# Kernel tuning notes

Measured on AMD Instinct MI355X. Metric: run time of the kernel, lower is better.

The kernel has to match this reference:

```python
import jax, jax.numpy as jnp
import numpy as np
from jax import lax

B, C_IN, C_OUT, H, W = 32, 96, 96, 56, 56
E = 8          # num_experts
HID = 576      # round(96 * 6)
K = 3          # depthwise kernel size


def setup_inputs() -> dict:
    key = jax.random.key(0)
    ks = jax.random.split(key, 12)
    f = lambda k, s, sc=0.05: jax.random.normal(k, s, dtype=jnp.float32) * sc
    return {
        "x": jax.random.normal(ks[0], (B, C_IN, H, W), dtype=jnp.float32),
        # router for expand conv (input = x, C_IN channels)
        "w_r1": f(ks[1], (E, C_IN)), "b_r1": jnp.zeros((E,), jnp.float32),
        # expert bank for 1x1 expand: [E, HID, C_IN]
        "w1": f(ks[2], (E, HID, C_IN)),
        "g1": jnp.ones((HID,), jnp.float32), "bt1": jnp.zeros((HID,), jnp.float32),
        "m1": f(ks[3], (HID,), 0.01), "v1": jax.random.uniform(ks[4], (HID,), dtype=jnp.float32) + 0.5,
        # router for depthwise conv (input = expanded features, HID channels)
        "w_r2": f(ks[5], (E, HID)), "b_r2": jnp.zeros((E,), jnp.float32),
        # expert bank for depthwise 3x3: [E, HID, K, K] (in/groups = 1)
        "w2": f(ks[6], (E, HID, K, K)),
        "g2": jnp.ones((HID,), jnp.float32), "bt2": jnp.zeros((HID,), jnp.float32),
        "m2": f(ks[7], (HID,), 0.01), "v2": jax.random.uniform(ks[8], (HID,), dtype=jnp.float32) + 0.5,
        # expert bank for 1x1 project: [E, C_OUT, HID]
        "w3": f(ks[9], (E, C_OUT, HID)),
        "g3": jnp.ones((C_OUT,), jnp.float32), "bt3": jnp.zeros((C_OUT,), jnp.float32),
        "m3": f(ks[10], (C_OUT,), 0.01), "v3": jax.random.uniform(ks[11], (C_OUT,), dtype=jnp.float32) + 0.5,
        # block-level router (input = x, C_IN channels) gating the project conv
        "w_r3": f(jax.random.fold_in(key, 99), (E, C_IN)), "b_r3": jnp.zeros((E,), jnp.float32),
    }


def _route(feat, Wf, bf):
    # BasicRouter: global avg pool -> Linear -> sigmoid. feat: [B, C, H, W] -> [B, E]
    return jax.nn.sigmoid(feat.mean(axis=(2, 3)) @ Wf.T + bf)


def _bn(y, g, b, m, v, eps=1e-5):
    inv = g * lax.rsqrt(v + eps)
    return y * inv[None, :, None, None] + (b - m * inv)[None, :, None, None]


def reference(x, w_r1, b_r1, w1, g1, bt1, m1, v1,
              w_r2, b_r2, w2, g2, bt2, m2, v2,
              w3, g3, bt3, m3, v3, w_r3, b_r3):
    r1 = _route(x, w_r1, b_r1)      # [B, E] gate for expand conv
    r_blk = _route(x, w_r3, b_r3)   # [B, E] block router gates project conv

    # --- CondConv 1x1 expand: per-sample mixed kernel as batched GEMM ---
    w1c = jnp.einsum('be,eoc->boc', r1, w1)              # [B, HID, C_IN]
    y = jnp.einsum('bchw,boc->bohw', x, w1c)             # [B, HID, H, W]
    y = jnp.clip(_bn(y, g1, bt1, m1, v1), 0.0, 6.0)      # ReLU6

    # --- CondConv depthwise 3x3 (groups = HID), router on expanded feats ---
    r2 = _route(y, w_r2, b_r2)                           # [B, E]
    kw = jnp.einsum('be,eckl->bckl', r2, w2).reshape(B * HID, 1, K, K)
    y = lax.conv_general_dilated(
        y.reshape(1, B * HID, H, W), kw, (1, 1), 'SAME',
        dimension_numbers=('NCHW', 'OIHW', 'NCHW'),
        feature_group_count=B * HID).reshape(B, HID, H, W)
    y = jnp.clip(_bn(y, g2, bt2, m2, v2), 0.0, 6.0)

    # --- CondConv 1x1 project, gated by the block router(x) ---
    w3c = jnp.einsum('be,eoc->boc', r_blk, w3)           # [B, C_OUT, HID]
    y = jnp.einsum('bchw,boc->bohw', y, w3c)             # [B, C_OUT, H, W]
    y = _bn(y, g3, bt3, m3, v3)

    return x + y  # stride==1 and inp==oup -> residual connection
```

## Files before the change

kernel.cpp:

```cpp
#include <hip/hip_runtime.h>
#include <hip/hip_bf16.h>

#define B_   32
#define CIN  96
#define COUT 96
#define NP   3136
#define NE   8
#define HIDD 576

typedef short bf16x8 __attribute__((ext_vector_type(8)));
typedef float f32x4 __attribute__((ext_vector_type(4)));

__device__ __forceinline__ unsigned short f2bf(float f) {
  __hip_bfloat16 h = __float2bfloat16(f);
  unsigned short u; __builtin_memcpy(&u, &h, 2); return u;
}
__device__ __forceinline__ float bf2f(unsigned short u) {
  unsigned int v = ((unsigned int)u) << 16;
  float f; __builtin_memcpy(&f, &v, 4); return f;
}
__device__ __forceinline__ float u2f(unsigned int v) {
  float f; __builtin_memcpy(&f, &v, 4); return f;
}

__global__ __launch_bounds__(256) void k_transpose(const float* __restrict__ x,
                                                   unsigned short* __restrict__ xt,
                                                   float* __restrict__ xpart) {
  __shared__ float tile[CIN][65];
  int bi = blockIdx.x; int b = bi / 49, pt = bi % 49; int p0 = pt * 64;
  int t = threadIdx.x;
  for (int j = t; j < CIN * 64; j += 256) {
    int c = j >> 6, pi = j & 63;
    tile[c][pi] = x[((size_t)(b * CIN + c)) * NP + p0 + pi];
  }
  __syncthreads();
  if (t < CIN) {
    float s = 0.f;
    for (int i = 0; i < 64; ++i) s += tile[t][i];
    xpart[((size_t)(b * 49 + pt)) * CIN + t] = s;
  }
  for (int j = t; j < 64 * CIN; j += 256) {
    int p = j / CIN, c = j % CIN;
    xt[((size_t)(b * NP + p0 + p)) * CIN + c] = f2bf(tile[c][p]);
  }
}

__global__ __launch_bounds__(64) void k_front(const float* __restrict__ xpart,
    const float* __restrict__ wr1, const float* __restrict__ br1,
    const float* __restrict__ wr3, const float* __restrict__ br3,
    float* __restrict__ r1, float* __restrict__ rblk,
    const float* g1, const float* bt1, const float* m1, const float* v1,
    const float* g2, const float* bt2, const float* m2, const float* v2,
    const float* g3, const float* bt3, const float* m3, const float* v3,
    float* sc1, float* bi1, float* sc2, float* bi2, float* sc3, float* bi3) {
  int bi = blockIdx.x; int lane = threadIdx.x;
  if (bi < 512) {
    const float* wr; const float* br; float* dst; int id;
    if (bi < 256) { wr = wr1; br = br1; dst = r1;   id = bi; }
    else          { wr = wr3; br = br3; dst = rblk; id = bi - 256; }
    int b = id >> 3, e = id & 7;
    float s = 0.f;
    for (int c = lane; c < CIN; c += 64) {
      const float* xp = xpart + (size_t)b * 49 * CIN + c;
      float xm = 0.f;
#pragma unroll 7
      for (int k = 0; k < 49; ++k) xm += xp[k * CIN];
      s += xm * (1.0f / NP) * wr[e * CIN + c];
    }
    s += __shfl_xor(s, 1);  s += __shfl_xor(s, 2);  s += __shfl_xor(s, 4);
    s += __shfl_xor(s, 8);  s += __shfl_xor(s, 16); s += __shfl_xor(s, 32);
    if (lane == 0) dst[id] = 1.0f / (1.0f + __expf(-(s + br[e])));
  } else {
    int i = (bi - 512) * 64 + lane;
    if (i < HIDD) {
      float s = g1[i] * rsqrtf(v1[i] + 1e-5f); sc1[i] = s; bi1[i] = bt1[i] - m1[i] * s;
    } else if (i < 2 * HIDD) {
      int c = i - HIDD;
      float s = g2[c] * rsqrtf(v2[c] + 1e-5f); sc2[c] = s; bi2[c] = bt2[c] - m2[c] * s;
    } else if (i < 2 * HIDD + COUT) {
      int c = i - 2 * HIDD;
      float s = g3[c] * rsqrtf(v3[c] + 1e-5f); sc3[c] = s; bi3[c] = bt3[c] - m3[c] * s;
    }
  }
}

__global__ __launch_bounds__(256) void k_mixw(
    const float* __restrict__ w1, const float* __restrict__ r1, unsigned short* __restrict__ w1c,
    const float* __restrict__ w3, const float* __restrict__ rblk, unsigned short* __restrict__ w3c) {
  __shared__ float rsh[256];
  int bi = blockIdx.x; int t = threadIdx.x;
  const float* w; const float* r; unsigned short* dst; int oc0;
  if (bi < 216) { w = w1; r = r1;   dst = w1c; oc0 = bi * 256; }
  else          { w = w3; r = rblk; dst = w3c; oc0 = (bi - 216) * 256; }
  rsh[t] = r[t];
  __syncthreads();
  int oc = oc0 + t;
  float wv[NE];
#pragma unroll
  for (int e = 0; e < NE; ++e) wv[e] = w[(size_t)e * 55296 + oc];
  for (int b = 0; b < B_; ++b) {
    float a = 0.f;
#pragma unroll
    for (int e = 0; e < NE; ++e) a += rsh[b * 8 + e] * wv[e];
    dst[(size_t)b * 55296 + oc] = f2bf(a);
  }
}

__global__ __launch_bounds__(256) void k_expand2(const unsigned short* __restrict__ xt,
    const unsigned short* __restrict__ w1c, const float* __restrict__ sc1,
    const float* __restrict__ bi1, unsigned short* __restrict__ y2,
    float* __restrict__ yspart) {
  __shared__ unsigned short As[64 * 104];
  __shared__ unsigned short Bs[64 * 104];
  int t = threadIdx.x;
  int pt = blockIdx.x;
  int p0 = pt * 64, o0 = blockIdx.y * 64, b = blockIdx.z;
  const unsigned short* ag = w1c + (size_t)b * 55296 + (size_t)o0 * 96;
  const unsigned short* bg = xt + ((size_t)b * NP + p0) * 96;
  for (int j = t; j < 768; j += 256) {
    int r = j / 12, ch = j % 12;
    *(int4*)(As + r * 104 + ch * 8) = *(const int4*)(ag + r * 96 + ch * 8);
    *(int4*)(Bs + r * 104 + ch * 8) = *(const int4*)(bg + r * 96 + ch * 8);
  }
  __syncthreads();
  int lane = t & 63, wv = t >> 6;
  int m = lane & 15, q = lane >> 4;
  f32x4 acc[4];
#pragma unroll
  for (int nt = 0; nt < 4; ++nt) acc[nt] = 0.f;
#pragma unroll
  for (int kk = 0; kk < 3; ++kk) {
    bf16x8 af = *(const bf16x8*)(As + (wv * 16 + m) * 104 + kk * 32 + q * 8);
#pragma unroll
    for (int nt = 0; nt < 4; ++nt) {
      bf16x8 bfb = *(const bf16x8*)(Bs + (nt * 16 + m) * 104 + kk * 32 + q * 8);
      acc[nt] = __builtin_amdgcn_mfma_f32_16x16x32_bf16(af, bfb, acc[nt], 0, 0, 0);
    }
  }
  __syncthreads();
  float sc[4], bb[4];
#pragma unroll
  for (int i = 0; i < 4; ++i) {
    int o = o0 + wv * 16 + q * 4 + i;
    sc[i] = sc1[o]; bb[i] = bi1[o];
  }
  float rs[4] = {0.f, 0.f, 0.f, 0.f};
  unsigned short* T = As;
#pragma unroll
  for (int nt = 0; nt < 4; ++nt) {
    unsigned short pk[4];
#pragma unroll
    for (int i = 0; i < 4; ++i) {
      float v = acc[nt][i] * sc[i] + bb[i];
      v = fminf(fmaxf(v, 0.f), 6.f);
      rs[i] += v;
      pk[i] = f2bf(v);
    }
    uint2 pv; __builtin_memcpy(&pv, pk, 8);
    *(uint2*)(T + (nt * 16 + m) * 72 + wv * 16 + q * 4) = pv;
  }
#pragma unroll
  for (int i = 0; i < 4; ++i) {
    float r = rs[i];
    r += __shfl_xor(r, 1); r += __shfl_xor(r, 2);
    r += __shfl_xor(r, 4); r += __shfl_xor(r, 8);
    if (m == 0)
      yspart[((size_t)b * 49 + pt) * HIDD + o0 + wv * 16 + q * 4 + i] = r;
  }
  __syncthreads();
  for (int j = t; j < 512; j += 256) {
    int r = j >> 3, ch = j & 7;
    *(int4*)(y2 + ((size_t)(b * NP + p0 + r)) * 576 + o0 + ch * 8) =
        *(const int4*)(T + r * 72 + ch * 8);
  }
}

__global__ __launch_bounds__(256) void k_mid(const float* __restrict__ yspart,
    const float* __restrict__ wr2, const float* __restrict__ br2,
    const float* __restrict__ w2, const float* __restrict__ sc2,
    const float* __restrict__ bi2, float* __restrict__ kwt) {
  __shared__ float ysum_l[HIDD];
  __shared__ float r2_l[NE];
  int b = blockIdx.x, t = threadIdx.x;
  const float* yp = yspart + (size_t)b * 49 * HIDD;
  for (int c = t; c < HIDD; c += 256) {
    float s = 0.f;
#pragma unroll 7
    for (int k = 0; k < 49; ++k) s += yp[k * HIDD + c];
    ysum_l[c] = s;
  }
  __syncthreads();
  int wv = t >> 6, lane = t & 63;
  for (int e = wv; e < NE; e += 4) {
    float s = 0.f;
    for (int h = lane; h < HIDD; h += 64)
      s += ysum_l[h] * (1.0f / NP) * wr2[e * HIDD + h];
    s += __shfl_xor(s, 1);  s += __shfl_xor(s, 2);  s += __shfl_xor(s, 4);
    s += __shfl_xor(s, 8);  s += __shfl_xor(s, 16); s += __shfl_xor(s, 32);
    if (lane == 0) r2_l[e] = 1.0f / (1.0f + __expf(-(s + br2[e])));
  }
  __syncthreads();
  float rr[NE];
#pragma unroll
  for (int e = 0; e < NE; ++e) rr[e] = r2_l[e];
  for (int c = t; c < HIDD; c += 256) {
    float sc = sc2[c];
    float* dst = kwt + (size_t)b * 5760 + c;
#pragma unroll
    for (int k = 0; k < 9; ++k) {
      float s = 0.f;
#pragma unroll
      for (int e = 0; e < NE; ++e) s += rr[e] * w2[((size_t)e * HIDD + c) * 9 + k];
      dst[k * 576] = s * sc;
    }
    dst[9 * 576] = bi2[c];
  }
}

__device__ __forceinline__ f32x4 cvt4(uint2 v) {
  f32x4 r;
  r[0] = u2f(v.x << 16); r[1] = u2f(v.x & 0xffff0000u);
  r[2] = u2f(v.y << 16); r[3] = u2f(v.y & 0xffff0000u);
  return r;
}
__device__ __forceinline__ uint2 pack4(f32x4 v) {
  uint2 r;
  r.x = (unsigned)f2bf(v[0]) | ((unsigned)f2bf(v[1]) << 16);
  r.y = (unsigned)f2bf(v[2]) | ((unsigned)f2bf(v[3]) << 16);
  return r;
}
__device__ __forceinline__ f32x4 clamp6(f32x4 v) {
#pragma unroll
  for (int i = 0; i < 4; ++i) v[i] = fminf(fmaxf(v[i], 0.f), 6.f);
  return v;
}

__global__ __launch_bounds__(256) void k_dwise5(const unsigned short* __restrict__ y2,
    const float* __restrict__ kwt, unsigned short* __restrict__ z2) {
  int id = blockIdx.x * 256 + threadIdx.x;
  int cg = id % 144; int rest = id / 144;
  int wh = rest & 1; rest >>= 1;
  int hp = rest % 28; int b = rest / 28;
  int c = cg * 4, h0 = hp * 2, wsrt = wh * 28;
  const float* kp = kwt + (size_t)b * 5760 + c;
  f32x4 tk[9], tb;
#pragma unroll
  for (int k = 0; k < 9; ++k) tk[k] = *(const f32x4*)(kp + k * 576);
  tb = *(const f32x4*)(kp + 9 * 576);
  bool ok0 = (hp > 0), ok3 = (hp < 27);
  int r0 = ok0 ? (h0 - 1) : h0;
  int r3 = ok3 ? (h0 + 2) : (h0 + 1);
  const unsigned short* rowp[4];
  rowp[0] = y2 + ((size_t)(b * NP + r0 * 56)) * 576 + c;
  rowp[1] = y2 + ((size_t)(b * NP + h0 * 56)) * 576 + c;
  rowp[2] = y2 + ((size_t)(b * NP + (h0 + 1) * 56)) * 576 + c;
  rowp[3] = y2 + ((size_t)(b * NP + r3 * 56)) * 576 + c;
  bool rok[4] = {ok0, true, true, ok3};
  unsigned short* zr0 = z2 + ((size_t)(b * NP + h0 * 56)) * 576 + c;
  unsigned short* zr1 = zr0 + (size_t)56 * 576;

  f32x4 P[4], C[4], N[4];

#define LOADCOL(D, col) do {                                           \
    _Pragma("unroll") for (int j = 0; j < 4; ++j) {                    \
      uint2 raw; raw.x = 0u; raw.y = 0u;                               \
      if ((unsigned)(col) < 56u && rok[j])                             \
        raw = *(const uint2*)(rowp[j] + (size_t)(col) * 576);          \
      D[j] = cvt4(raw);                                                \
    } } while (0)

#define DSTEP(PP, CC, NN, wcur) do {                                   \
    f32x4 o0 = tb, o1 = tb;                                            \
    _Pragma("unroll") for (int jj = 0; jj < 3; ++jj) {                 \
      o0 += PP[jj] * tk[jj * 3] + CC[jj] * tk[jj * 3 + 1] + NN[jj] * tk[jj * 3 + 2]; \
      o1 += PP[jj + 1] * tk[jj * 3] + CC[jj + 1] * tk[jj * 3 + 1] + NN[jj + 1] * tk[jj * 3 + 2]; \
    }                                                                  \
    *(uint2*)(zr0 + (size_t)(wcur) * 576) = pack4(clamp6(o0));         \
    *(uint2*)(zr1 + (size_t)(wcur) * 576) = pack4(clamp6(o1));         \
    LOADCOL(PP, (wcur) + 2);                                           \
  } while (0)

  LOADCOL(P, wsrt - 1);
  LOADCOL(C, wsrt);
  LOADCOL(N, wsrt + 1);
  for (int w = wsrt; w < wsrt + 27; w += 3) {
    DSTEP(P, C, N, w);
    DSTEP(C, N, P, w + 1);
    DSTEP(N, P, C, w + 2);
  }
  DSTEP(P, C, N, wsrt + 27);
#undef DSTEP
#undef LOADCOL
}

__global__ __launch_bounds__(384) void k_project4(const unsigned short* __restrict__ z2,
    const unsigned short* __restrict__ w3c, const float* __restrict__ sc3,
    const float* __restrict__ bi3, const float* __restrict__ x, float* __restrict__ out) {
  __shared__ unsigned short As[96 * 72];
  __shared__ unsigned short Bs[112 * 72];
  int t = threadIdx.x;
  int p0 = blockIdx.x * 112, b = blockIdx.z;
  const unsigned short* ag = w3c + (size_t)b * 55296;
  const unsigned short* zb = z2 + ((size_t)(b * NP + p0)) * 576;
  int lane = t & 63, wv = t >> 6;
  int m = lane & 15, q = lane >> 4;
  f32x4 acc[7];
#pragma unroll
  for (int nt = 0; nt < 7; ++nt) acc[nt] = 0.f;
  for (int c0 = 0; c0 < HIDD; c0 += 64) {
    __syncthreads();
    for (int j = t; j < 768; j += 384) {
      int r = j >> 3, ch = j & 7;
      *(int4*)(As + r * 72 + ch * 8) = *(const int4*)(ag + (size_t)r * 576 + c0 + ch * 8);
    }
    for (int j = t; j < 896; j += 384) {
      int r = j >> 3, ch = j & 7;
      *(int4*)(Bs + r * 72 + ch * 8) = *(const int4*)(zb + (size_t)r * 576 + c0 + ch * 8);
    }
    __syncthreads();
#pragma unroll
    for (int kk = 0; kk < 2; ++kk) {
      bf16x8 af = *(const bf16x8*)(As + (wv * 16 + m) * 72 + kk * 32 + q * 8);
#pragma unroll
      for (int nt = 0; nt < 7; ++nt) {
        bf16x8 bfb = *(const bf16x8*)(Bs + (nt * 16 + m) * 72 + kk * 32 + q * 8);
        acc[nt] = __builtin_amdgcn_mfma_f32_16x16x32_bf16(af, bfb, acc[nt], 0, 0, 0);
      }
    }
  }
#pragma unroll
  for (int i = 0; i < 4; ++i) {
    int o = wv * 16 + q * 4 + i;
    float sc = sc3[o], bb = bi3[o];
    size_t base = ((size_t)(b * COUT + o)) * NP + p0;
#pragma unroll
    for (int nt = 0; nt < 7; ++nt) {
      float v = acc[nt][i] * sc + bb + x[base + nt * 16 + m];
      out[base + nt * 16 + m] = v;
    }
  }
}

#define OFF_XT     ((size_t)0)
#define OFF_KWT    OFF_XT
#define OFF_Y      ((size_t)19267584)
#define OFF_Z      ((size_t)134873088)
#define OFF_XPART  OFF_Z
#define OFF_YSPART (OFF_Z + 602112)
#define OFF_W1C    ((size_t)250478592)
#define OFF_W3C    ((size_t)254017536)
#define OFF_R1     ((size_t)257642496)
#define OFF_RBLK   ((size_t)257643520)
#define OFF_SC1    ((size_t)257645568)
#define OFF_BI1    ((size_t)257647872)
#define OFF_SC2    ((size_t)257650176)
#define OFF_BI2    ((size_t)257652480)
#define OFF_SC3    ((size_t)257654784)
#define OFF_BI3    ((size_t)257655168)

extern "C" void kernel_launch(void* const* d_in, const int* in_sizes, int n_in,
                              void* d_out, int out_size, void* d_ws, size_t ws_size,
                              hipStream_t stream) {
  const float* x   = (const float*)d_in[0];
  const float* wr1 = (const float*)d_in[1];
  const float* br1 = (const float*)d_in[2];
  const float* w1  = (const float*)d_in[3];
  const float* g1  = (const float*)d_in[4];
  const float* bt1 = (const float*)d_in[5];
  const float* m1  = (const float*)d_in[6];
  const float* v1  = (const float*)d_in[7];
  const float* wr2 = (const float*)d_in[8];
  const float* br2 = (const float*)d_in[9];
  const float* w2  = (const float*)d_in[10];
  const float* g2  = (const float*)d_in[11];
  const float* bt2 = (const float*)d_in[12];
  const float* m2  = (const float*)d_in[13];
  const float* v2  = (const float*)d_in[14];
  const float* w3  = (const float*)d_in[15];
  const float* g3  = (const float*)d_in[16];
  const float* bt3 = (const float*)d_in[17];
  const float* m3  = (const float*)d_in[18];
  const float* v3  = (const float*)d_in[19];
  const float* wr3 = (const float*)d_in[20];
  const float* br3 = (const float*)d_in[21];
  float* out = (float*)d_out;
  char* ws = (char*)d_ws;

  unsigned short* xt     = (unsigned short*)(ws + OFF_XT);
  unsigned short* y2     = (unsigned short*)(ws + OFF_Y);
  unsigned short* z2     = (unsigned short*)(ws + OFF_Z);
  unsigned short* w1c    = (unsigned short*)(ws + OFF_W1C);
  unsigned short* w3c    = (unsigned short*)(ws + OFF_W3C);
  float* xpart  = (float*)(ws + OFF_XPART);
  float* yspart = (float*)(ws + OFF_YSPART);
  float* r1     = (float*)(ws + OFF_R1);
  float* rblk   = (float*)(ws + OFF_RBLK);
  float* sc1    = (float*)(ws + OFF_SC1);
  float* bi1    = (float*)(ws + OFF_BI1);
  float* sc2    = (float*)(ws + OFF_SC2);
  float* bi2    = (float*)(ws + OFF_BI2);
  float* sc3    = (float*)(ws + OFF_SC3);
  float* bi3    = (float*)(ws + OFF_BI3);
  float* kwt    = (float*)(ws + OFF_KWT);

  k_transpose<<<32 * 49, 256, 0, stream>>>(x, xt, xpart);
  k_front<<<532, 64, 0, stream>>>(xpart, wr1, br1, wr3, br3, r1, rblk,
                                  g1, bt1, m1, v1, g2, bt2, m2, v2, g3, bt3, m3, v3,
                                  sc1, bi1, sc2, bi2, sc3, bi3);
  k_mixw<<<432, 256, 0, stream>>>(w1, r1, w1c, w3, rblk, w3c);
  k_expand2<<<dim3(49, 9, 32), 256, 0, stream>>>(xt, w1c, sc1, bi1, y2, yspart);
  k_mid<<<32, 256, 0, stream>>>(yspart, wr2, br2, w2, sc2, bi2, kwt);
  k_dwise5<<<1008, 256, 0, stream>>>(y2, kwt, z2);
  k_project4<<<dim3(28, 1, 32), 384, 0, stream>>>(z2, w3c, sc3, bi3, x, out);
}
```

Before: 322.5 us.

## Retile project GEMM to 64-pixel tiles with register-prefetched double buffering

```diff
diff --git a/kernel.cpp b/kernel.cpp
--- a/kernel.cpp
+++ b/kernel.cpp
@@ -293,50 +293,89 @@
 #undef LOADCOL
 }
 
-__global__ __launch_bounds__(384) void k_project4(const unsigned short* __restrict__ z2,
+__global__ __launch_bounds__(256) void k_project5(const unsigned short* __restrict__ z2,
     const unsigned short* __restrict__ w3c, const float* __restrict__ sc3,
     const float* __restrict__ bi3, const float* __restrict__ x, float* __restrict__ out) {
   __shared__ unsigned short As[96 * 72];
-  __shared__ unsigned short Bs[112 * 72];
+  __shared__ unsigned short Bs[64 * 72];
   int t = threadIdx.x;
-  int p0 = blockIdx.x * 112, b = blockIdx.z;
+  int p0 = blockIdx.x * 64, b = blockIdx.z;
   const unsigned short* ag = w3c + (size_t)b * 55296;
   const unsigned short* zb = z2 + ((size_t)(b * NP + p0)) * 576;
   int lane = t & 63, wv = t >> 6;
+  int wr = wv >> 1, wc = wv & 1;
   int m = lane & 15, q = lane >> 4;
-  f32x4 acc[7];
-#pragma unroll
-  for (int nt = 0; nt < 7; ++nt) acc[nt] = 0.f;
-  for (int c0 = 0; c0 < HIDD; c0 += 64) {
+  int rr0 = t >> 3, ch0 = t & 7;
+
+  f32x4 acc[3][2];
+#pragma unroll
+  for (int a = 0; a < 3; ++a)
+#pragma unroll
+    for (int nt = 0; nt < 2; ++nt) acc[a][nt] = 0.f;
+
+  int4 ra0, ra1, ra2, rb0, rb1;
+
+#define LOADT(c0) do {                                                          \
+    ra0 = *(const int4*)(ag + (size_t)(rr0)      * 576 + (c0) + ch0 * 8);       \
+    ra1 = *(const int4*)(ag + (size_t)(rr0 + 32) * 576 + (c0) + ch0 * 8);       \
+    ra2 = *(const int4*)(ag + (size_t)(rr0 + 64) * 576 + (c0) + ch0 * 8);       \
+    rb0 = *(const int4*)(zb + (size_t)(rr0)      * 576 + (c0) + ch0 * 8);       \
+    rb1 = *(const int4*)(zb + (size_t)(rr0 + 32) * 576 + (c0) + ch0 * 8);       \
+  } while (0)
+
+#define WRITET() do {                                                           \
+    *(int4*)(As + (rr0)      * 72 + ch0 * 8) = ra0;                             \
+    *(int4*)(As + (rr0 + 32) * 72 + ch0 * 8) = ra1;                             \
+    *(int4*)(As + (rr0 + 64) * 72 + ch0 * 8) = ra2;                             \
+    *(int4*)(Bs + (rr0)      * 72 + ch0 * 8) = rb0;                             \
+    *(int4*)(Bs + (rr0 + 32) * 72 + ch0 * 8) = rb1;                             \
+  } while (0)
+
+#define COMPUTE() do {                                                          \
+    _Pragma("unroll") for (int kk = 0; kk < 2; ++kk) {                          \
+      bf16x8 af0 = *(const bf16x8*)(As + (wr * 48 +  0 + m) * 72 + kk * 32 + q * 8); \
+      bf16x8 af1 = *(const bf16x8*)(As + (wr * 48 + 16 + m) * 72 + kk * 32 + q * 8); \
+      bf16x8 af2 = *(const bf16x8*)(As + (wr * 48 + 32 + m) * 72 + kk * 32 + q * 8); \
+      bf16x8 bf0 = *(const bf16x8*)(Bs + (wc * 32 +  0 + m) * 72 + kk * 32 + q * 8); \
+      bf16x8 bf1 = *(const bf16x8*)(Bs + (wc * 32 + 16 + m) * 72 + kk * 32 + q * 8); \
+      acc[0][0] = __builtin_amdgcn_mfma_f32_16x16x32_bf16(af0, bf0, acc[0][0], 0, 0, 0); \
+      acc[0][1] = __builtin_amdgcn_mfma_f32_16x16x32_bf16(af0, bf1, acc[0][1], 0, 0, 0); \
+      acc[1][0] = __builtin_amdgcn_mfma_f32_16x16x32_bf16(af1, bf0, acc[1][0], 0, 0, 0); \
+      acc[1][1] = __builtin_amdgcn_mfma_f32_16x16x32_bf16(af1, bf1, acc[1][1], 0, 0, 0); \
+      acc[2][0] = __builtin_amdgcn_mfma_f32_16x16x32_bf16(af2, bf0, acc[2][0], 0, 0, 0); \
+      acc[2][1] = __builtin_amdgcn_mfma_f32_16x16x32_bf16(af2, bf1, acc[2][1], 0, 0, 0); \
+    } } while (0)
+
+  LOADT(0);
+  WRITET();
+  __syncthreads();
+
+#pragma unroll 1
+  for (int tt = 0; tt < 8; ++tt) {
+    LOADT((tt + 1) * 64);
+    COMPUTE();
     __syncthreads();
-    for (int j = t; j < 768; j += 384) {
-      int r = j >> 3, ch = j & 7;
-      *(int4*)(As + r * 72 + ch * 8) = *(const int4*)(ag + (size_t)r * 576 + c0 + ch * 8);
-    }
-    for (int j = t; j < 896; j += 384) {
-      int r = j >> 3, ch = j & 7;
-      *(int4*)(Bs + r * 72 + ch * 8) = *(const int4*)(zb + (size_t)r * 576 + c0 + ch * 8);
-    }
+    WRITET();
     __syncthreads();
-#pragma unroll
-    for (int kk = 0; kk < 2; ++kk) {
-      bf16x8 af = *(const bf16x8*)(As + (wv * 16 + m) * 72 + kk * 32 + q * 8);
-#pragma unroll
-      for (int nt = 0; nt < 7; ++nt) {
-        bf16x8 bfb = *(const bf16x8*)(Bs + (nt * 16 + m) * 72 + kk * 32 + q * 8);
-        acc[nt] = __builtin_amdgcn_mfma_f32_16x16x32_bf16(af, bfb, acc[nt], 0, 0, 0);
+  }
+  COMPUTE();
+
+#undef LOADT
+#undef WRITET
+#undef COMPUTE
+
+#pragma unroll
+  for (int a = 0; a < 3; ++a) {
+#pragma unroll
+    for (int i = 0; i < 4; ++i) {
+      int o = wr * 48 + a * 16 + q * 4 + i;
+      float sc = sc3[o], bb = bi3[o];
+      size_t base = ((size_t)(b * COUT + o)) * NP + p0 + wc * 32;
+#pragma unroll
+      for (int nt = 0; nt < 2; ++nt) {
+        float v = acc[a][nt][i] * sc + bb + x[base + nt * 16 + m];
+        out[base + nt * 16 + m] = v;
       }
-    }
-  }
-#pragma unroll
-  for (int i = 0; i < 4; ++i) {
-    int o = wv * 16 + q * 4 + i;
-    float sc = sc3[o], bb = bi3[o];
-    size_t base = ((size_t)(b * COUT + o)) * NP + p0;
-#pragma unroll
-    for (int nt = 0; nt < 7; ++nt) {
-      float v = acc[nt][i] * sc + bb + x[base + nt * 16 + m];
-      out[base + nt * 16 + m] = v;
     }
   }
 }
@@ -411,5 +450,5 @@
   k_expand2<<<dim3(49, 9, 32), 256, 0, stream>>>(xt, w1c, sc1, bi1, y2, yspart);
   k_mid<<<32, 256, 0, stream>>>(yspart, wr2, br2, w2, sc2, bi2, kwt);
   k_dwise5<<<1008, 256, 0, stream>>>(y2, kwt, z2);
-  k_project4<<<dim3(28, 1, 32), 384, 0, stream>>>(z2, w3c, sc3, bi3, x, out);
-}
+  k_project5<<<dim3(49, 1, 32), 256, 0, stream>>>(z2, w3c, sc3, bi3, x, out);
+}
```

Result: faster. 314.8 us (-2.4%).

## Fuse depthwise 3x3 conv into project GEMM via per-row LDS tile

Applied to the files above, without the earlier changes.

```diff
diff --git a/kernel.cpp b/kernel.cpp
--- a/kernel.cpp
+++ b/kernel.cpp
@@ -14,10 +14,6 @@
 __device__ __forceinline__ unsigned short f2bf(float f) {
   __hip_bfloat16 h = __float2bfloat16(f);
   unsigned short u; __builtin_memcpy(&u, &h, 2); return u;
-}
-__device__ __forceinline__ float bf2f(unsigned short u) {
-  unsigned int v = ((unsigned int)u) << 16;
-  float f; __builtin_memcpy(&f, &v, 4); return f;
 }
 __device__ __forceinline__ float u2f(unsigned int v) {
   float f; __builtin_memcpy(&f, &v, 4); return f;
@@ -235,109 +231,136 @@
   return v;
 }
 
-__global__ __launch_bounds__(256) void k_dwise5(const unsigned short* __restrict__ y2,
-    const float* __restrict__ kwt, unsigned short* __restrict__ z2) {
-  int id = blockIdx.x * 256 + threadIdx.x;
-  int cg = id % 144; int rest = id / 144;
-  int wh = rest & 1; rest >>= 1;
-  int hp = rest % 28; int b = rest / 28;
-  int c = cg * 4, h0 = hp * 2, wsrt = wh * 28;
-  const float* kp = kwt + (size_t)b * 5760 + c;
-  f32x4 tk[9], tb;
-#pragma unroll
-  for (int k = 0; k < 9; ++k) tk[k] = *(const f32x4*)(kp + k * 576);
-  tb = *(const f32x4*)(kp + 9 * 576);
-  bool ok0 = (hp > 0), ok3 = (hp < 27);
-  int r0 = ok0 ? (h0 - 1) : h0;
-  int r3 = ok3 ? (h0 + 2) : (h0 + 1);
-  const unsigned short* rowp[4];
-  rowp[0] = y2 + ((size_t)(b * NP + r0 * 56)) * 576 + c;
-  rowp[1] = y2 + ((size_t)(b * NP + h0 * 56)) * 576 + c;
-  rowp[2] = y2 + ((size_t)(b * NP + (h0 + 1) * 56)) * 576 + c;
-  rowp[3] = y2 + ((size_t)(b * NP + r3 * 56)) * 576 + c;
-  bool rok[4] = {ok0, true, true, ok3};
-  unsigned short* zr0 = z2 + ((size_t)(b * NP + h0 * 56)) * 576 + c;
-  unsigned short* zr1 = zr0 + (size_t)56 * 576;
-
-  f32x4 P[4], C[4], N[4];
-
-#define LOADCOL(D, col) do {                                           \
-    _Pragma("unroll") for (int j = 0; j < 4; ++j) {                    \
-      uint2 raw; raw.x = 0u; raw.y = 0u;                               \
-      if ((unsigned)(col) < 56u && rok[j])                             \
-        raw = *(const uint2*)(rowp[j] + (size_t)(col) * 576);          \
-      D[j] = cvt4(raw);                                                \
+__global__ __launch_bounds__(512, 4) void k_dwproj(const unsigned short* __restrict__ y2,
+    const float* __restrict__ kwt, const unsigned short* __restrict__ w3c,
+    const float* __restrict__ sc3, const float* __restrict__ bi3,
+    const float* __restrict__ x, float* __restrict__ out) {
+  __shared__ unsigned short zl[56 * 584];
+  __shared__ unsigned short As[96 * 72];
+  int t = threadIdx.x;
+  int h = blockIdx.x, b = blockIdx.z;
+  const unsigned short* ag = w3c + (size_t)b * 55296;
+
+  int r0 = t >> 3, c8 = t & 7;
+  int r1 = 64 + (t >> 3);
+  bool two = (t < 256);
+  int4 ra0, ra1;
+#define LOADA(kc) do {                                                       \
+    ra0 = *(const int4*)(ag + (size_t)r0 * 576 + (kc) * 64 + c8 * 8);        \
+    if (two) ra1 = *(const int4*)(ag + (size_t)r1 * 576 + (kc) * 64 + c8 * 8); \
+  } while (0)
+#define WRITEA() do {                                                        \
+    *(int4*)(As + r0 * 72 + c8 * 8) = ra0;                                   \
+    if (two) *(int4*)(As + r1 * 72 + c8 * 8) = ra1;                          \
+  } while (0)
+
+  LOADA(0);
+
+  {
+    bool okU = (h > 0), okD = (h < 55);
+    int rU = okU ? (h - 1) : h;
+    int rD = okD ? (h + 1) : h;
+    f32x4 d0, d1, d2;
+#pragma unroll 1
+    for (int task = t; task < 576; task += 512) {
+      int cgi = task % 144;
+      int seg = task / 144;
+      int c = cgi * 4, w0 = seg * 14;
+      const float* kp = kwt + (size_t)b * 5760 + c;
+      f32x4 tk[9], tb;
+#pragma unroll
+      for (int k = 0; k < 9; ++k) tk[k] = *(const f32x4*)(kp + k * 576);
+      tb = *(const f32x4*)(kp + 9 * 576);
+      const unsigned short* yrU = y2 + ((size_t)(b * NP + rU * 56)) * 576 + c;
+      const unsigned short* yrC = y2 + ((size_t)(b * NP + h  * 56)) * 576 + c;
+      const unsigned short* yrD = y2 + ((size_t)(b * NP + rD * 56)) * 576 + c;
+
+#define LOADC3(j) do {                                                       \
+      uint2 q0, q1, q2;                                                      \
+      q0.x = q0.y = q1.x = q1.y = q2.x = q2.y = 0u;                          \
+      if ((unsigned)(j) < 56u) {                                             \
+        if (okU) q0 = *(const uint2*)(yrU + (size_t)(j) * 576);              \
+        q1 = *(const uint2*)(yrC + (size_t)(j) * 576);                       \
+        if (okD) q2 = *(const uint2*)(yrD + (size_t)(j) * 576);              \
+      }                                                                      \
+      d0 = cvt4(q0); d1 = cvt4(q1); d2 = cvt4(q2);                           \
+    } while (0)
+
+#define SCAT3(A, Bv, Cv, j, STORE) do {                                      \
+      LOADC3(j);                                                             \
+      A  += d0 * tk[2] + d1 * tk[5] + d2 * tk[8];                            \
+      Bv += d0 * tk[1] + d1 * tk[4] + d2 * tk[7];                            \
+      Cv += d0 * tk[0] + d1 * tk[3] + d2 * tk[6];                            \
+      if (STORE)                                                             \
+        *(uint2*)(zl + (size_t)((j) - 1) * 584 + c) = pack4(clamp6(A));      \
+      A = tb;                                                                \
+    } while (0)
+
+      f32x4 Av = tb, Bv = tb, Cv = tb;
+      SCAT3(Av, Bv, Cv, w0 - 1, false);
+      SCAT3(Bv, Cv, Av, w0,     false);
+#pragma unroll 1
+      for (int u = 0; u < 4; ++u) {
+        int j = w0 + 1 + u * 3;
+        SCAT3(Cv, Av, Bv, j,     true);
+        SCAT3(Av, Bv, Cv, j + 1, true);
+        SCAT3(Bv, Cv, Av, j + 2, true);
+      }
+      SCAT3(Cv, Av, Bv, w0 + 13, true);
+      LOADC3(w0 + 14);
+      Av += d0 * tk[2] + d1 * tk[5] + d2 * tk[8];
+      *(uint2*)(zl + (size_t)(w0 + 13) * 584 + c) = pack4(clamp6(Av));
+#undef SCAT3
+#undef LOADC3
+    }
+  }
+
+  WRITEA();
+  __syncthreads();
+
+  int lane = t & 63, wv = t >> 6;
+  int wr = wv >> 2, wc = wv & 3;
+  int m = lane & 15, q = lane >> 4;
+  int px = wc * 16 + m;
+  int pxr = (px < 56) ? px : 55;
+  f32x4 acc0, acc1, acc2;
+  acc0 = 0.f; acc1 = 0.f; acc2 = 0.f;
+
+#define COMPUTE(kc) do {                                                     \
+    _Pragma("unroll") for (int kk = 0; kk < 2; ++kk) {                       \
+      bf16x8 bfv = *(const bf16x8*)(zl + (size_t)pxr * 584 + (kc) * 64 + kk * 32 + q * 8); \
+      bf16x8 af0 = *(const bf16x8*)(As + (wr * 48 +  0 + m) * 72 + kk * 32 + q * 8); \
+      bf16x8 af1 = *(const bf16x8*)(As + (wr * 48 + 16 + m) * 72 + kk * 32 + q * 8); \
+      bf16x8 af2 = *(const bf16x8*)(As + (wr * 48 + 32 + m) * 72 + kk * 32 + q * 8); \
+      acc0 = __builtin_amdgcn_mfma_f32_16x16x32_bf16(af0, bfv, acc0, 0, 0, 0); \
+      acc1 = __builtin_amdgcn_mfma_f32_16x16x32_bf16(af1, bfv, acc1, 0, 0, 0); \
+      acc2 = __builtin_amdgcn_mfma_f32_16x16x32_bf16(af2, bfv, acc2, 0, 0, 0); \
     } } while (0)
 
-#define DSTEP(PP, CC, NN, wcur) do {                                   \
-    f32x4 o0 = tb, o1 = tb;                                            \
-    _Pragma("unroll") for (int jj = 0; jj < 3; ++jj) {                 \
-      o0 += PP[jj] * tk[jj * 3] + CC[jj] * tk[jj * 3 + 1] + NN[jj] * tk[jj * 3 + 2]; \
-      o1 += PP[jj + 1] * tk[jj * 3] + CC[jj + 1] * tk[jj * 3 + 1] + NN[jj + 1] * tk[jj * 3 + 2]; \
-    }                                                                  \
-    *(uint2*)(zr0 + (size_t)(wcur) * 576) = pack4(clamp6(o0));         \
-    *(uint2*)(zr1 + (size_t)(wcur) * 576) = pack4(clamp6(o1));         \
-    LOADCOL(PP, (wcur) + 2);                                           \
-  } while (0)
-
-  LOADCOL(P, wsrt - 1);
-  LOADCOL(C, wsrt);
-  LOADCOL(N, wsrt + 1);
-  for (int w = wsrt; w < wsrt + 27; w += 3) {
-    DSTEP(P, C, N, w);
-    DSTEP(C, N, P, w + 1);
-    DSTEP(N, P, C, w + 2);
-  }
-  DSTEP(P, C, N, wsrt + 27);
-#undef DSTEP
-#undef LOADCOL
-}
-
-__global__ __launch_bounds__(384) void k_project4(const unsigned short* __restrict__ z2,
-    const unsigned short* __restrict__ w3c, const float* __restrict__ sc3,
-    const float* __restrict__ bi3, const float* __restrict__ x, float* __restrict__ out) {
-  __shared__ unsigned short As[96 * 72];
-  __shared__ unsigned short Bs[112 * 72];
-  int t = threadIdx.x;
-  int p0 = blockIdx.x * 112, b = blockIdx.z;
-  const unsigned short* ag = w3c + (size_t)b * 55296;
-  const unsigned short* zb = z2 + ((size_t)(b * NP + p0)) * 576;
-  int lane = t & 63, wv = t >> 6;
-  int m = lane & 15, q = lane >> 4;
-  f32x4 acc[7];
-#pragma unroll
-  for (int nt = 0; nt < 7; ++nt) acc[nt] = 0.f;
-  for (int c0 = 0; c0 < HIDD; c0 += 64) {
+#pragma unroll 1
+  for (int kc = 0; kc < 8; ++kc) {
+    LOADA(kc + 1);
+    COMPUTE(kc);
     __syncthreads();
-    for (int j = t; j < 768; j += 384) {
-      int r = j >> 3, ch = j & 7;
-      *(int4*)(As + r * 72 + ch * 8) = *(const int4*)(ag + (size_t)r * 576 + c0 + ch * 8);
-    }
-    for (int j = t; j < 896; j += 384) {
-      int r = j >> 3, ch = j & 7;
-      *(int4*)(Bs + r * 72 + ch * 8) = *(const int4*)(zb + (size_t)r * 576 + c0 + ch * 8);
-    }
+    WRITEA();
     __syncthreads();
-#pragma unroll
-    for (int kk = 0; kk < 2; ++kk) {
-      bf16x8 af = *(const bf16x8*)(As + (wv * 16 + m) * 72 + kk * 32 + q * 8);
-#pragma unroll
-      for (int nt = 0; nt < 7; ++nt) {
-        bf16x8 bfb = *(const bf16x8*)(Bs + (nt * 16 + m) * 72 + kk * 32 + q * 8);
-        acc[nt] = __builtin_amdgcn_mfma_f32_16x16x32_bf16(af, bfb, acc[nt], 0, 0, 0);
-      }
-    }
-  }
-#pragma unroll
-  for (int i = 0; i < 4; ++i) {
-    int o = wv * 16 + q * 4 + i;
-    float sc = sc3[o], bb = bi3[o];
-    size_t base = ((size_t)(b * COUT + o)) * NP + p0;
-#pragma unroll
-    for (int nt = 0; nt < 7; ++nt) {
-      float v = acc[nt][i] * sc + bb + x[base + nt * 16 + m];
-      out[base + nt * 16 + m] = v;
-    }
+  }
+  COMPUTE(8);
+
+#undef COMPUTE
+#undef LOADA
+#undef WRITEA
+
+  if (px < 56) {
+    size_t pbase = (size_t)b * COUT * NP + (size_t)h * 56 + px;
+#define EPI(ACC, a) do {                                                     \
+    _Pragma("unroll") for (int i = 0; i < 4; ++i) {                          \
+      int o = wr * 48 + (a) * 16 + q * 4 + i;                                \
+      size_t idx = pbase + (size_t)o * NP;                                   \
+      out[idx] = ACC[i] * sc3[o] + bi3[o] + x[idx];                          \
+    } } while (0)
+    EPI(acc0, 0); EPI(acc1, 1); EPI(acc2, 2);
+#undef EPI
   }
 }
 
@@ -388,7 +411,6 @@
 
   unsigned short* xt     = (unsigned short*)(ws + OFF_XT);
   unsigned short* y2     = (unsigned short*)(ws + OFF_Y);
-  unsigned short* z2     = (unsigned short*)(ws + OFF_Z);
   unsigned short* w1c    = (unsigned short*)(ws + OFF_W1C);
   unsigned short* w3c    = (unsigned short*)(ws + OFF_W3C);
   float* xpart  = (float*)(ws + OFF_XPART);
@@ -410,6 +432,5 @@
   k_mixw<<<432, 256, 0, stream>>>(w1, r1, w1c, w3, rblk, w3c);
   k_expand2<<<dim3(49, 9, 32), 256, 0, stream>>>(xt, w1c, sc1, bi1, y2, yspart);
   k_mid<<<32, 256, 0, stream>>>(yspart, wr2, br2, w2, sc2, bi2, kwt);
-  k_dwise5<<<1008, 256, 0, stream>>>(y2, kwt, z2);
-  k_project4<<<dim3(28, 1, 32), 384, 0, stream>>>(z2, w3c, sc3, bi3, x, out);
-}
+  k_dwproj<<<dim3(56, 1, 32), 512, 0, stream>>>(y2, kwt, w3c, sc3, bi3, x, out);
+}
```

Result: faster. 300.9 us (-6.7%).
